# Kernel optimization log

Measured on AMD Instinct MI355X. Metric: run time of the kernel, lower is better.

## Reference

```python
import jax, jax.numpy as jnp
import numpy as np

BETA = 0.25
NUM_SEMANTIC = 8192
EPS = 1e-8  # torch F.normalize / cosine_similarity eps


def _normalize(v, axis=-1):
    n = jnp.linalg.norm(v, axis=axis, keepdims=True)
    return v / jnp.maximum(n, EPS)


def _cos_sim(a, b):
    # faithful to F.cosine_similarity(a, b, dim=-1)
    na = jnp.maximum(jnp.linalg.norm(a, axis=-1), EPS)
    nb = jnp.maximum(jnp.linalg.norm(b, axis=-1), EPS)
    return jnp.sum(a * b, axis=-1) / (na * nb)


def setup_inputs() -> dict:
    key = jax.random.key(0)
    k1, k2, k3 = jax.random.split(key, 3)
    x = jax.random.normal(k1, (8192, 1024), dtype=jnp.float32)
    semantic_embeddings = jax.random.normal(k2, (8192, 1024), dtype=jnp.float32)
    # trunc_normal_(std=0.02) ~ clipped normal; plain scaled normal is a fine init stand-in
    learnable_entries = 0.02 * jax.random.normal(k3, (128, 1024), dtype=jnp.float32)
    return {"x": x, "semantic_embeddings": semantic_embeddings,
            "learnable_entries": learnable_entries}


def reference(x, semantic_embeddings, learnable_entries):
    frozen = _normalize(semantic_embeddings)          # [S, D] (buffer, pre-normalized)
    learned = _normalize(learnable_entries)           # [L, D]
    codebook = jnp.concatenate([frozen, learned], 0)  # [S+L, D]

    xn = _normalize(x)                                # [N, D]
    logits = xn @ codebook.T                          # [N, S+L]
    indices = jnp.argmax(logits, axis=-1)             # [N]
    z_q = codebook[indices]                           # [N, D]
    z_q_st = xn + jax.lax.stop_gradient(z_q - xn)

    is_learnable = (indices >= NUM_SEMANTIC).astype(jnp.float32)
    commitment_loss = jnp.mean(1.0 - _cos_sim(xn, jax.lax.stop_gradient(z_q)))
    per_token = 1.0 - _cos_sim(jax.lax.stop_gradient(xn), z_q)
    vq_loss = jnp.sum(per_token * is_learnable) / (jnp.sum(is_learnable) + 1e-6)
    quant_loss = vq_loss + BETA * commitment_loss

    return logits, indices, z_q, z_q_st, vq_loss, commitment_loss, quant_loss
```

## Files before the change

kernel.cpp:

```cpp
#include <hip/hip_runtime.h>
#include <stdint.h>


#define N_TOK   8192
#define DIM     1024
#define N_SEM   8192
#define N_LEARN 128
#define N_CODE  (N_SEM + N_LEARN)

typedef _Float16 f16;
typedef _Float16 f16x4 __attribute__((ext_vector_type(4)));
typedef _Float16 f16x8 __attribute__((ext_vector_type(8)));
typedef float    f32x4 __attribute__((ext_vector_type(4)));

__global__ __launch_bounds__(256) void k_prep(
    const float* __restrict__ x,   float* __restrict__ invnx,
    f16* __restrict__ xHi,  f16* __restrict__ xLo,
    const float* __restrict__ sem, float* __restrict__ invnb,
    f16* __restrict__ semHi, f16* __restrict__ semLo,
    const float* __restrict__ lrn,
    f16* __restrict__ lrnHi, f16* __restrict__ lrnLo,
    unsigned long long* __restrict__ keys)
{
    const int b = blockIdx.x;
    const int t = threadIdx.x;
    const float* in; float* invn; f16* hi; f16* lo; int row;
    if (b < N_TOK) {
        row = b; in = x; invn = invnx; hi = xHi; lo = xLo;
        if (t == 0) keys[row] = 0ULL;
    } else if (b < N_TOK + N_SEM) {
        row = b - N_TOK; in = sem; invn = invnb; hi = semHi; lo = semLo;
    } else {
        row = b - N_TOK - N_SEM; in = lrn; invn = invnb + N_SEM;
        hi = lrnHi; lo = lrnLo;
    }

    float4 v = ((const float4*)(in + (size_t)row * DIM))[t];
    float ss = v.x*v.x + v.y*v.y + v.z*v.z + v.w*v.w;
    #pragma unroll
    for (int off = 32; off > 0; off >>= 1) ss += __shfl_xor(ss, off);
    __shared__ float red[4];
    if ((t & 63) == 0) red[t >> 6] = ss;

    f16 h0 = (f16)v.x, h1 = (f16)v.y, h2 = (f16)v.z, h3 = (f16)v.w;
    f16x4 hv = {h0, h1, h2, h3};
    f16x4 lv = {(f16)(v.x - (float)h0), (f16)(v.y - (float)h1),
                (f16)(v.z - (float)h2), (f16)(v.w - (float)h3)};
    ((f16x4*)(hi + (size_t)row * DIM))[t] = hv;
    ((f16x4*)(lo + (size_t)row * DIM))[t] = lv;

    __syncthreads();
    if (t == 0) {
        float tot = red[0] + red[1] + red[2] + red[3];
        invn[row] = 1.f / fmaxf(sqrtf(tot), 1e-8f);
    }
}

#define BM 128
#define BN 128
#define BK 32

__device__ __forceinline__ void gload16(const void* g, void* l) {
    __builtin_amdgcn_global_load_lds(
        (const __attribute__((address_space(1))) void*)g,
        (__attribute__((address_space(3))) void*)l, 16, 0, 0);
}

__global__ __launch_bounds__(256) void k_gemm_mfma(
    const f16* __restrict__ xHi,  const f16* __restrict__ xLo,
    const f16* __restrict__ semHi, const f16* __restrict__ semLo,
    const f16* __restrict__ lrnHi, const f16* __restrict__ lrnLo,
    const float* __restrict__ invnx, const float* __restrict__ invnb,
    float* __restrict__ logits, unsigned long long* __restrict__ keys)
{
    __shared__ __align__(16) f16 sA[2][BM * BK];
    __shared__ __align__(16) f16 sB[2][BN * BK];

    const int t    = threadIdx.x;
    const int lane = t & 63;
    const int wid  = t >> 6;
    const int row0 = blockIdx.x * BM;
    const int col0 = blockIdx.y * BN;
    const int wm   = (wid >> 1) * 64;
    const int wn   = (wid & 1) * 64;

    const f16* bh; const f16* blo;
    if (col0 < N_SEM) { bh = semHi + (size_t)col0 * DIM;
                        blo = semLo + (size_t)col0 * DIM; }
    else              { bh = lrnHi + (size_t)(col0 - N_SEM) * DIM;
                        blo = lrnLo + (size_t)(col0 - N_SEM) * DIM; }
    const f16* ah  = xHi + (size_t)row0 * DIM;
    const f16* alo = xLo + (size_t)row0 * DIM;

    const int sr = t >> 2;
    const int sc = (t & 3) ^ ((sr >> 1) & 3);
    const size_t g0 = (size_t)sr * DIM + sc * 8;
    const size_t g1 = g0 + (size_t)64 * DIM;

    const int fr  = lane & 15;
    const int fg  = lane >> 4;
    const int swz = fg ^ ((fr >> 1) & 3);

    const f16* aLb = alo + (size_t)(wm + fr) * DIM + fg * 8;
    const f16* bLb = blo + (size_t)(wn + fr) * DIM + fg * 8;

    f32x4 acc[4][4];
    #pragma unroll
    for (int i = 0; i < 4; ++i)
        #pragma unroll
        for (int j = 0; j < 4; ++j) acc[i][j] = (f32x4)0.f;

#define STAGE(b, k0) do { \
        gload16(ah + g0 + (k0), &sA[b][t * 8]); \
        gload16(ah + g1 + (k0), &sA[b][t * 8 + 2048]); \
        gload16(bh + g0 + (k0), &sB[b][t * 8]); \
        gload16(bh + g1 + (k0), &sB[b][t * 8 + 2048]); \
    } while (0)

    STAGE(0, 0);
    asm volatile("s_waitcnt vmcnt(0)" ::: "memory");
    __builtin_amdgcn_s_barrier();

    int cur = 0;
    #pragma unroll 1
    for (int k0 = 0; k0 < DIM; k0 += BK) {
        f16x8 aL[4], bL[4];
        #pragma unroll
        for (int f = 0; f < 4; ++f) {
            aL[f] = *(const f16x8*)(aLb + (size_t)f * 16 * DIM + k0);
            bL[f] = *(const f16x8*)(bLb + (size_t)f * 16 * DIM + k0);
        }
        if (k0 + BK < DIM) STAGE(cur ^ 1, k0 + BK);

        f16x8 aH[4], bH[4];
        #pragma unroll
        for (int f = 0; f < 4; ++f) {
            aH[f] = *(const f16x8*)(&sA[cur][(wm + f * 16 + fr) * BK + swz * 8]);
            bH[f] = *(const f16x8*)(&sB[cur][(wn + f * 16 + fr) * BK + swz * 8]);
        }
        #pragma unroll
        for (int i = 0; i < 4; ++i)
            #pragma unroll
            for (int j = 0; j < 4; ++j)
                acc[i][j] = __builtin_amdgcn_mfma_f32_16x16x32_f16(aH[i], bH[j], acc[i][j], 0, 0, 0);
        #pragma unroll
        for (int i = 0; i < 4; ++i)
            #pragma unroll
            for (int j = 0; j < 4; ++j) {
                acc[i][j] = __builtin_amdgcn_mfma_f32_16x16x32_f16(aH[i], bL[j], acc[i][j], 0, 0, 0);
                acc[i][j] = __builtin_amdgcn_mfma_f32_16x16x32_f16(aL[i], bH[j], acc[i][j], 0, 0, 0);
            }

        asm volatile("s_waitcnt vmcnt(0)" ::: "memory");
        __builtin_amdgcn_s_barrier();
        cur ^= 1;
    }
#undef STAGE

    float ibv[4];
    #pragma unroll
    for (int fn = 0; fn < 4; ++fn) ibv[fn] = invnb[col0 + wn + fn * 16 + fr];

    #pragma unroll
    for (int fm = 0; fm < 4; ++fm) {
        #pragma unroll
        for (int reg = 0; reg < 4; ++reg) {
            const int row = row0 + wm + fm * 16 + fg * 4 + reg;
            const float ia = invnx[row];
            float best = -3.4e38f; int bcol = 0;
            float* dst = logits + (size_t)row * N_CODE + col0 + wn + fr;
            #pragma unroll
            for (int fn = 0; fn < 4; ++fn) {
                float v = acc[fm][fn][reg] * (ia * ibv[fn]);
                dst[fn * 16] = v;
                int c = col0 + wn + fn * 16 + fr;
                if (v > best) { best = v; bcol = c; }
            }
            #pragma unroll
            for (int off = 8; off > 0; off >>= 1) {
                float ov = __shfl_xor(best, off);
                int   oc = __shfl_xor(bcol, off);
                if (ov > best || (ov == best && oc < bcol)) { best = ov; bcol = oc; }
            }
            if (fr == 0) {
                unsigned int u = __float_as_uint(best);
                unsigned int s = (u & 0x80000000u) ? ~u : (u | 0x80000000u);
                unsigned long long key = ((unsigned long long)s << 14) |
                                         (unsigned long long)(16383 - bcol);
                atomicMax(keys + row, key);
            }
        }
    }
}

__global__ __launch_bounds__(256) void k_epilogue(
    const float* __restrict__ X,
    const float* __restrict__ SEM,
    const float* __restrict__ LRN,
    const float* __restrict__ invnx,
    const float* __restrict__ invnb,
    const unsigned long long* __restrict__ keys,
    float* __restrict__ o_idx,
    float* __restrict__ o_zq,
    float* __restrict__ o_zst,
    float* __restrict__ perTok)
{
    const int tok = blockIdx.x;
    const int t = threadIdx.x;
    const int col = 16383 - (int)(keys[tok] & 16383ULL);
    const float ix = invnx[tok];
    const float ib = invnb[col];
    const float* crow = (col < N_SEM) ? (SEM + (size_t)col * DIM)
                                      : (LRN + (size_t)(col - N_SEM) * DIM);

    float4 xr = ((const float4*)(X + (size_t)tok * DIM))[t];
    float4 cr = ((const float4*)crow)[t];
    float4 xv; xv.x = xr.x*ix; xv.y = xr.y*ix; xv.z = xr.z*ix; xv.w = xr.w*ix;
    float4 zv; zv.x = cr.x*ib; zv.y = cr.y*ib; zv.z = cr.z*ib; zv.w = cr.w*ib;

    float d  = xv.x*zv.x + xv.y*zv.y + xv.z*zv.z + xv.w*zv.w;
    float nx = xv.x*xv.x + xv.y*xv.y + xv.z*xv.z + xv.w*xv.w;
    float nz = zv.x*zv.x + zv.y*zv.y + zv.z*zv.z + zv.w*zv.w;
    #pragma unroll
    for (int off = 32; off > 0; off >>= 1) {
        d  += __shfl_xor(d, off);
        nx += __shfl_xor(nx, off);
        nz += __shfl_xor(nz, off);
    }
    __shared__ float rd[4], rx[4], rz[4];
    if ((t & 63) == 0) { rd[t>>6] = d; rx[t>>6] = nx; rz[t>>6] = nz; }
    __syncthreads();

    float4 zs;
    zs.x = xv.x + (zv.x - xv.x);
    zs.y = xv.y + (zv.y - xv.y);
    zs.z = xv.z + (zv.z - xv.z);
    zs.w = xv.w + (zv.w - xv.w);
    ((float4*)o_zq)[(size_t)tok * 256 + t] = zv;
    ((float4*)o_zst)[(size_t)tok * 256 + t] = zs;

    if (t == 0) {
        float D  = rd[0]+rd[1]+rd[2]+rd[3];
        float NX = rx[0]+rx[1]+rx[2]+rx[3];
        float NZ = rz[0]+rz[1]+rz[2]+rz[3];
        float cs = D / (fmaxf(sqrtf(NX), 1e-8f) * fmaxf(sqrtf(NZ), 1e-8f));
        o_idx[tok]  = (float)col;
        perTok[tok] = 1.f - cs;
    }
}

__global__ __launch_bounds__(256) void k_final(
    const float* __restrict__ perTok,
    const float* __restrict__ o_idx,
    float* __restrict__ o_scal)
{
    const int t = threadIdx.x;
    float cs = 0.f, vs = 0.f, vc = 0.f;
    for (int i = t; i < N_TOK; i += 256) {
        float p = perTok[i];
        cs += p;
        if (o_idx[i] >= (float)N_SEM) { vs += p; vc += 1.f; }
    }
    #pragma unroll
    for (int off = 32; off > 0; off >>= 1) {
        cs += __shfl_xor(cs, off);
        vs += __shfl_xor(vs, off);
        vc += __shfl_xor(vc, off);
    }
    __shared__ float r0[4], r1[4], r2[4];
    if ((t & 63) == 0) { r0[t>>6] = cs; r1[t>>6] = vs; r2[t>>6] = vc; }
    __syncthreads();
    if (t == 0) {
        float C = r0[0]+r0[1]+r0[2]+r0[3];
        float V = r1[0]+r1[1]+r1[2]+r1[3];
        float K = r2[0]+r2[1]+r2[2]+r2[3];
        float commit = C / (float)N_TOK;
        float vq     = V / (K + 1e-6f);
        o_scal[0] = vq;
        o_scal[1] = commit;
        o_scal[2] = vq + 0.25f * commit;
    }
}

extern "C" void kernel_launch(void* const* d_in, const int* in_sizes, int n_in,
                              void* d_out, int out_size, void* d_ws, size_t ws_size,
                              hipStream_t stream) {
    const float* x   = (const float*)d_in[0];
    const float* sem = (const float*)d_in[1];
    const float* lrn = (const float*)d_in[2];

    float* invnx = (float*)d_ws;
    float* invnb = invnx + N_TOK;
    unsigned long long* keys = (unsigned long long*)(invnb + N_CODE);
    float* perTok = (float*)(keys + N_TOK);
    f16* lrnHi = (f16*)(perTok + N_TOK);
    f16* lrnLo = lrnHi + (size_t)N_LEARN * DIM;

    float* out      = (float*)d_out;
    float* o_logits = out;
    float* o_idx    = o_logits + (size_t)N_TOK * N_CODE;
    float* o_zq     = o_idx + N_TOK;
    float* o_zst    = o_zq + (size_t)N_TOK * DIM;
    float* o_scal   = o_zst + (size_t)N_TOK * DIM;

    f16* xHi   = (f16*)o_zq;
    f16* xLo   = xHi + (size_t)N_TOK * DIM;
    f16* semHi = (f16*)o_zst;
    f16* semLo = semHi + (size_t)N_SEM * DIM;

    k_prep<<<N_TOK + N_SEM + N_LEARN, 256, 0, stream>>>(
        x, invnx, xHi, xLo, sem, invnb, semHi, semLo, lrn, lrnHi, lrnLo, keys);

    dim3 g2(N_TOK / BM, N_CODE / BN);
    k_gemm_mfma<<<g2, 256, 0, stream>>>(xHi, xLo, semHi, semLo, lrnHi, lrnLo,
                                        invnx, invnb, o_logits, keys);

    k_epilogue<<<N_TOK, 256, 0, stream>>>(x, sem, lrn, invnx, invnb, keys,
                                          o_idx, o_zq, o_zst, perTok);
    k_final<<<1, 256, 0, stream>>>(perTok, o_idx, o_scal);
}
```

Before: 1.005 ms.

## Stage low-part fragments through LDS, swizzle block order, raise MFMA priority

Instead of reading the lo-precision A/B fragments straight from global memory in every k-step, the kernel now loads hi and lo tiles into double-buffered LDS with async global-to-LDS loads and reads all four fragment sets from shared memory. It also remaps workgroup IDs with a modulo-8 swizzle, meant to spread neighbouring tiles across XCDs for cache locality, and wraps the MFMA block in s_setprio. LDS use doubles to 64 KB per block, which may reduce occupancy, and the barrier changes from an explicit vmcnt wait to __syncthreads.

```diff
diff --git a/kernel.cpp b/kernel.cpp
--- a/kernel.cpp
+++ b/kernel.cpp
@@ -73,16 +73,24 @@
     const float* __restrict__ invnx, const float* __restrict__ invnb,
     float* __restrict__ logits, unsigned long long* __restrict__ keys)
 {
-    __shared__ __align__(16) f16 sA[2][BM * BK];
-    __shared__ __align__(16) f16 sB[2][BN * BK];
+    __shared__ __align__(16) f16 sAh[2][BM * BK];
+    __shared__ __align__(16) f16 sAl[2][BM * BK];
+    __shared__ __align__(16) f16 sBh[2][BN * BK];
+    __shared__ __align__(16) f16 sBl[2][BN * BK];
 
     const int t    = threadIdx.x;
     const int lane = t & 63;
     const int wid  = t >> 6;
-    const int row0 = blockIdx.x * BM;
-    const int col0 = blockIdx.y * BN;
     const int wm   = (wid >> 1) * 64;
     const int wn   = (wid & 1) * 64;
+
+    const int nwg  = (N_TOK / BM) * (N_CODE / BN);
+    const int bid  = blockIdx.y * (N_TOK / BM) + blockIdx.x;
+    const int swzb = (bid % 8) * (nwg / 8) + bid / 8;
+    const int rb   = swzb % (N_TOK / BM);
+    const int cb   = swzb / (N_TOK / BM);
+    const int row0 = rb * BM;
+    const int col0 = cb * BN;
 
     const f16* bh; const f16* blo;
     if (col0 < N_SEM) { bh = semHi + (size_t)col0 * DIM;
@@ -101,58 +109,51 @@
     const int fg  = lane >> 4;
     const int swz = fg ^ ((fr >> 1) & 3);
 
-    const f16* aLb = alo + (size_t)(wm + fr) * DIM + fg * 8;
-    const f16* bLb = blo + (size_t)(wn + fr) * DIM + fg * 8;
-
     f32x4 acc[4][4];
     #pragma unroll
     for (int i = 0; i < 4; ++i)
         #pragma unroll
         for (int j = 0; j < 4; ++j) acc[i][j] = (f32x4)0.f;
 
-#define STAGE(b, k0) do { \
-        gload16(ah + g0 + (k0), &sA[b][t * 8]); \
-        gload16(ah + g1 + (k0), &sA[b][t * 8 + 2048]); \
-        gload16(bh + g0 + (k0), &sB[b][t * 8]); \
-        gload16(bh + g1 + (k0), &sB[b][t * 8 + 2048]); \
+#define STAGE(bf, k0) do { \
+        gload16(ah  + g0 + (k0), &sAh[bf][t * 8]); \
+        gload16(ah  + g1 + (k0), &sAh[bf][t * 8 + 2048]); \
+        gload16(alo + g0 + (k0), &sAl[bf][t * 8]); \
+        gload16(alo + g1 + (k0), &sAl[bf][t * 8 + 2048]); \
+        gload16(bh  + g0 + (k0), &sBh[bf][t * 8]); \
+        gload16(bh  + g1 + (k0), &sBh[bf][t * 8 + 2048]); \
+        gload16(blo + g0 + (k0), &sBl[bf][t * 8]); \
+        gload16(blo + g1 + (k0), &sBl[bf][t * 8 + 2048]); \
     } while (0)
 
     STAGE(0, 0);
-    asm volatile("s_waitcnt vmcnt(0)" ::: "memory");
-    __builtin_amdgcn_s_barrier();
+    __syncthreads();
 
     int cur = 0;
     #pragma unroll 1
     for (int k0 = 0; k0 < DIM; k0 += BK) {
-        f16x8 aL[4], bL[4];
+        if (k0 + BK < DIM) STAGE(cur ^ 1, k0 + BK);
+
+        f16x8 aH[4], aL[4], bH[4], bL[4];
         #pragma unroll
         for (int f = 0; f < 4; ++f) {
-            aL[f] = *(const f16x8*)(aLb + (size_t)f * 16 * DIM + k0);
-            bL[f] = *(const f16x8*)(bLb + (size_t)f * 16 * DIM + k0);
+            aH[f] = *(const f16x8*)(&sAh[cur][(wm + f * 16 + fr) * BK + swz * 8]);
+            aL[f] = *(const f16x8*)(&sAl[cur][(wm + f * 16 + fr) * BK + swz * 8]);
+            bH[f] = *(const f16x8*)(&sBh[cur][(wn + f * 16 + fr) * BK + swz * 8]);
+            bL[f] = *(const f16x8*)(&sBl[cur][(wn + f * 16 + fr) * BK + swz * 8]);
         }
-        if (k0 + BK < DIM) STAGE(cur ^ 1, k0 + BK);
-
-        f16x8 aH[4], bH[4];
-        #pragma unroll
-        for (int f = 0; f < 4; ++f) {
-            aH[f] = *(const f16x8*)(&sA[cur][(wm + f * 16 + fr) * BK + swz * 8]);
-            bH[f] = *(const f16x8*)(&sB[cur][(wn + f * 16 + fr) * BK + swz * 8]);
-        }
-        #pragma unroll
-        for (int i = 0; i < 4; ++i)
-            #pragma unroll
-            for (int j = 0; j < 4; ++j)
-                acc[i][j] = __builtin_amdgcn_mfma_f32_16x16x32_f16(aH[i], bH[j], acc[i][j], 0, 0, 0);
+        __builtin_amdgcn_s_setprio(1);
         #pragma unroll
         for (int i = 0; i < 4; ++i)
             #pragma unroll
             for (int j = 0; j < 4; ++j) {
+                acc[i][j] = __builtin_amdgcn_mfma_f32_16x16x32_f16(aH[i], bH[j], acc[i][j], 0, 0, 0);
                 acc[i][j] = __builtin_amdgcn_mfma_f32_16x16x32_f16(aH[i], bL[j], acc[i][j], 0, 0, 0);
                 acc[i][j] = __builtin_amdgcn_mfma_f32_16x16x32_f16(aL[i], bH[j], acc[i][j], 0, 0, 0);
             }
-
-        asm volatile("s_waitcnt vmcnt(0)" ::: "memory");
-        __builtin_amdgcn_s_barrier();
+        __builtin_amdgcn_s_setprio(0);
+
+        __syncthreads();
         cur ^= 1;
     }
 #undef STAGE
```

Result: faster. 877.3 us (-12.7%).
